# Kernel optimization log

Hardware: AMD Instinct MI355X
Metric: run time of the kernel (lower is better)

## Reference

```python
import jax, jax.numpy as jnp
import numpy as np

N_NODES = 50000
N_EDGES = 800000
IN_DIM = 128
HIDDEN = 128
N_GRAPHS = 64


def setup_inputs() -> dict:
    key = jax.random.key(0)
    ks = jax.random.split(key, 16)
    x = jax.random.normal(ks[0], (N_NODES, IN_DIM), dtype=jnp.float32)
    edge_index = jax.random.randint(ks[1], (2, N_EDGES), 0, N_NODES, dtype=jnp.int64)
    batch = jnp.sort(jax.random.randint(ks[2], (N_NODES,), 0, N_GRAPHS, dtype=jnp.int64))
    s = 1.0 / np.sqrt(IN_DIM)
    sh = 1.0 / np.sqrt(HIDDEN)
    return {
        "x": x,
        "edge_index": edge_index,
        "batch": batch,
        # SAGEConv1: lin_l (on aggregated neighbors, with bias), lin_r (on root, no bias)
        "w1l": jax.random.uniform(ks[3], (HIDDEN, IN_DIM), jnp.float32, -s, s),
        "b1l": jax.random.uniform(ks[4], (HIDDEN,), jnp.float32, -s, s),
        "w1r": jax.random.uniform(ks[5], (HIDDEN, IN_DIM), jnp.float32, -s, s),
        # SAGEConv2
        "w2l": jax.random.uniform(ks[6], (HIDDEN, HIDDEN), jnp.float32, -sh, sh),
        "b2l": jax.random.uniform(ks[7], (HIDDEN,), jnp.float32, -sh, sh),
        "w2r": jax.random.uniform(ks[8], (HIDDEN, HIDDEN), jnp.float32, -sh, sh),
        # MLP head
        "wl1": jax.random.uniform(ks[9], (64, HIDDEN), jnp.float32, -sh, sh),
        "bl1": jax.random.uniform(ks[10], (64,), jnp.float32, -sh, sh),
        "wout": jax.random.uniform(ks[11], (1, 64), jnp.float32, -0.125, 0.125),
        "bout": jax.random.uniform(ks[12], (1,), jnp.float32, -0.125, 0.125),
    }


def _sage_conv(x, src, dst, wl, bl, wr, n_nodes):
    # PyG SAGEConv (aggr='mean'): out = lin_l(mean_{j in N(i)} x_j) + lin_r(x_i)
    agg = jax.ops.segment_sum(x[src], dst, num_segments=n_nodes)  # [N, d]
    deg = jax.ops.segment_sum(jnp.ones_like(dst, dtype=x.dtype), dst, num_segments=n_nodes)
    agg = agg / jnp.maximum(deg, 1.0)[:, None]
    return agg @ wl.T + bl + x @ wr.T


def reference(x, edge_index, batch, w1l, b1l, w1r, w2l, b2l, w2r, wl1, bl1, wout, bout):
    src, dst = edge_index[0], edge_index[1]
    n = x.shape[0]
    h = jax.nn.relu(_sage_conv(x, src, dst, w1l, b1l, w1r, n))
    h = jax.nn.relu(_sage_conv(h, src, dst, w2l, b2l, w2r, n))
    # global_mean_pool over graph ids in `batch` -> [G, hidden]
    sums = jax.ops.segment_sum(h, batch, num_segments=N_GRAPHS)
    cnt = jax.ops.segment_sum(jnp.ones((n,), h.dtype), batch, num_segments=N_GRAPHS)
    g = sums / jnp.maximum(cnt, 1.0)[:, None]
    # MLP head (dropout is identity in eval mode)
    g = jax.nn.relu(g @ wl1.T + bl1)
    return jax.nn.sigmoid(g @ wout.T + bout)  # [G, 1]
```

## Files before the change

kernel.cpp:

```cpp
#include <hip/hip_runtime.h>
#include <cstdint>
#include <cstddef>

#define N_NODES  50000
#define N_EDGES  800000
#define DIM      128
#define N_GRAPHS 64
#define NB       98
#define BSH      9
#define EPB      2048
#define BPAD     16
#define CAP      16384

typedef __attribute__((ext_vector_type(8))) short     bf16x8;
typedef __attribute__((ext_vector_type(4))) float     f32x4;

__device__ __forceinline__ int clamp_node(int v) {
    return v < 0 ? 0 : (v >= N_NODES ? N_NODES - 1 : v);
}
__device__ __forceinline__ unsigned short f2bf(float f) {
    union { float f; unsigned u; } v; v.f = f;
    unsigned r = v.u + 0x7FFF + ((v.u >> 16) & 1);
    return (unsigned short)(r >> 16);
}
__device__ __forceinline__ float bflo(unsigned u) {
    union { unsigned u; float f; } v; v.u = u << 16; return v.f;
}
__device__ __forceinline__ float bfhi(unsigned u) {
    union { unsigned u; float f; } v; v.u = u & 0xFFFF0000u; return v.f;
}

__global__ __launch_bounds__(512) void k_bucket(const int* __restrict__ ei,
                                                int* __restrict__ bcur,
                                                unsigned* __restrict__ tmp) {
    __shared__ int cnt[128], cur[128], ofs[128];
    __shared__ int s[512];
    __shared__ unsigned list[EPB];
    int t = threadIdx.x;
    int base = blockIdx.x * EPB;
    int eend = base + EPB; if (eend > N_EDGES) eend = N_EDGES;

    if (t < 128) cnt[t] = 0;
    __syncthreads();

    int d[4], sv[4];
    bool ok[4];
    #pragma unroll
    for (int i = 0; i < 4; ++i) {
        int e = base + t + i * 512;
        ok[i] = (e < eend);
        if (ok[i]) {
            d[i]  = clamp_node(ei[N_EDGES + e]);
            sv[i] = clamp_node(ei[e]);
            atomicAdd(&cnt[d[i] >> BSH], 1);
        }
    }
    __syncthreads();
    int v = (t < 128) ? cnt[t] : 0;
    s[t] = v;
    __syncthreads();
    for (int off = 1; off < 128; off <<= 1) {
        int y = (t >= off && t < 128) ? s[t - off] : 0;
        __syncthreads();
        if (t < 128) s[t] += y;
        __syncthreads();
    }
    if (t < 128) { ofs[t] = s[t] - v; cur[t] = s[t] - v; }
    __syncthreads();
    #pragma unroll
    for (int i = 0; i < 4; ++i) {
        if (ok[i]) {
            int b = d[i] >> BSH;
            int p = atomicAdd(&cur[b], 1);
            list[p] = (unsigned)sv[i] | ((unsigned)(d[i] & 511) << 16);
        }
    }
    __syncthreads();
    int wv = t >> 6, lane = t & 63;
    const int NGRP = 13;
    for (int jj = 0; jj < NGRP; ++jj) {
        int b = wv + 8 * ((jj + (int)blockIdx.x) % NGRP);
        if (b >= NB) continue;
        int c = cnt[b];
        if (c == 0) continue;
        int gpos;
        if (lane == 0) gpos = atomicAdd(&bcur[b * BPAD], c);
        gpos = __shfl(gpos, 0);
        if (gpos + c > CAP) c = (gpos < CAP) ? (CAP - gpos) : 0;
        int ls = ofs[b];
        for (int i = lane; i < c; i += 64) tmp[b * CAP + gpos + i] = list[ls + i];
    }
}

__global__ __launch_bounds__(512) void k_csr(const unsigned* __restrict__ tmp,
                                             const int* __restrict__ bcur,
                                             int2* __restrict__ rsse,
                                             int* __restrict__ srcs) {
    __shared__ int lh[512], lcur[512];
    __shared__ int s[512];
    int b = blockIdx.x;
    int t = threadIdx.x;
    int base = b * CAP;
    int nc = bcur[b * BPAD];
    if (nc > CAP) nc = CAP;

    lh[t] = 0;
    __syncthreads();
    for (int e = t; e < nc; e += 512)
        atomicAdd(&lh[tmp[base + e] >> 16], 1);
    __syncthreads();
    int v = lh[t];
    s[t] = v;
    __syncthreads();
    for (int off = 1; off < 512; off <<= 1) {
        int y = (t >= off) ? s[t - off] : 0;
        __syncthreads();
        s[t] += y;
        __syncthreads();
    }
    int st = s[t] - v;
    lcur[t] = st;
    int node = (b << BSH) + t;
    if (node < N_NODES) rsse[node] = make_int2(base + st, base + st + v);
    __syncthreads();
    for (int e = t; e < nc; e += 512) {
        unsigned val = tmp[base + e];
        int pos = atomicAdd(&lcur[val >> 16], 1);
        srcs[base + pos] = (int)(val & 0xFFFFu);
    }
}

__global__ __launch_bounds__(256) void k_prep(const float* __restrict__ x,
                                              unsigned short* __restrict__ xb,
                                              const float* __restrict__ W1l,
                                              const float* __restrict__ W1r,
                                              const float* __restrict__ W2l,
                                              const float* __restrict__ W2r,
                                              unsigned short* __restrict__ wbuf1,
                                              unsigned short* __restrict__ wbuf2) {
    int i = blockIdx.x * 256 + threadIdx.x;
    const int n8 = N_NODES * 16;
    if (i < n8) {
        const float4* p = (const float4*)(x + (size_t)i * 8);
        float4 a = p[0], b = p[1];
        union { unsigned short s[8]; uint4 u; } o;
        o.s[0] = f2bf(a.x); o.s[1] = f2bf(a.y); o.s[2] = f2bf(a.z); o.s[3] = f2bf(a.w);
        o.s[4] = f2bf(b.x); o.s[5] = f2bf(b.y); o.s[6] = f2bf(b.z); o.s[7] = f2bf(b.w);
        *(uint4*)(xb + (size_t)i * 8) = o.u;
        return;
    }
    int tid = i - n8;
    if (tid >= 2 * 8 * 8 * 64) return;
    int which = tid >> 12;
    int id    = tid & 4095;
    const float* Wl = which ? W2l : W1l;
    const float* Wr = which ? W2r : W1r;
    unsigned short* wbuf = which ? wbuf2 : wbuf1;
    int lane = id & 63;
    int ks   = (id >> 6) & 7;
    int ot   = id >> 9;
    int o  = ot * 16 + (lane & 15);
    int kb = ks * 32 + ((lane >> 4) << 3);
    union { unsigned short s[8]; uint4 u; } frag;
    #pragma unroll
    for (int j = 0; j < 8; ++j) {
        int k = kb + j;
        float v = (k < DIM) ? Wl[o * DIM + k] : Wr[o * DIM + (k - DIM)];
        frag.s[j] = f2bf(v);
    }
    *(uint4*)(wbuf + (size_t)id * 8) = frag.u;
}

__global__ __launch_bounds__(256) void k_sage(const unsigned short* __restrict__ feat,
                                              const unsigned short* __restrict__ in2b,
                                              const int2* __restrict__ rsse,
                                              const int* __restrict__ srcs,
                                              const unsigned short* __restrict__ wbuf,
                                              const float* __restrict__ bias,
                                              unsigned short* __restrict__ outb) {
    __shared__ unsigned short almp[16][136];
    int t    = threadIdx.x;
    int wave = t >> 6;
    int lane = t & 63;
    int n0   = blockIdx.x * 16;

    bf16x8 B[2][8];
    #pragma unroll
    for (int ot = 0; ot < 2; ++ot)
        #pragma unroll
        for (int ks = 0; ks < 8; ++ks)
            B[ot][ks] = *(const bf16x8*)(wbuf +
                (((size_t)(wave * 2 + ot) * 8 + ks) * 64 + lane) * 8);

    {
        int q   = lane >> 4;
        int sub = lane & 15;
        int node  = n0 + wave * 4 + q;
        int2 se   = rsse[node];
        int start = se.x;
        int end   = se.y;
        float a0 = 0.f, a1 = 0.f, a2 = 0.f, a3 = 0.f;
        float a4 = 0.f, a5 = 0.f, a6 = 0.f, a7 = 0.f;
        const size_t coff = (size_t)sub * 8;

#define ACC8(r) { a0 += bflo(r.x); a1 += bfhi(r.x); a2 += bflo(r.y); a3 += bfhi(r.y); \
                  a4 += bflo(r.z); a5 += bfhi(r.z); a6 += bflo(r.w); a7 += bfhi(r.w); }
        int e = start;
        for (; e + 8 <= end; e += 8) {
            uint4 r0 = *(const uint4*)(feat + (size_t)srcs[e + 0] * DIM + coff);
            uint4 r1 = *(const uint4*)(feat + (size_t)srcs[e + 1] * DIM + coff);
            uint4 r2 = *(const uint4*)(feat + (size_t)srcs[e + 2] * DIM + coff);
            uint4 r3 = *(const uint4*)(feat + (size_t)srcs[e + 3] * DIM + coff);
            uint4 r4 = *(const uint4*)(feat + (size_t)srcs[e + 4] * DIM + coff);
            uint4 r5 = *(const uint4*)(feat + (size_t)srcs[e + 5] * DIM + coff);
            uint4 r6 = *(const uint4*)(feat + (size_t)srcs[e + 6] * DIM + coff);
            uint4 r7 = *(const uint4*)(feat + (size_t)srcs[e + 7] * DIM + coff);
            ACC8(r0) ACC8(r1) ACC8(r2) ACC8(r3) ACC8(r4) ACC8(r5) ACC8(r6) ACC8(r7)
        }
        for (; e + 2 <= end; e += 2) {
            uint4 r0 = *(const uint4*)(feat + (size_t)srcs[e + 0] * DIM + coff);
            uint4 r1 = *(const uint4*)(feat + (size_t)srcs[e + 1] * DIM + coff);
            ACC8(r0) ACC8(r1)
        }
        if (e < end) {
            uint4 r0 = *(const uint4*)(feat + (size_t)srcs[e] * DIM + coff);
            ACC8(r0)
        }
#undef ACC8
        float inv = 1.0f / fmaxf((float)(end - start), 1.0f);
        union { unsigned short s[8]; uint4 u; } o;
        o.s[0] = f2bf(a0 * inv); o.s[1] = f2bf(a1 * inv);
        o.s[2] = f2bf(a2 * inv); o.s[3] = f2bf(a3 * inv);
        o.s[4] = f2bf(a4 * inv); o.s[5] = f2bf(a5 * inv);
        o.s[6] = f2bf(a6 * inv); o.s[7] = f2bf(a7 * inv);
        *(uint4*)&almp[wave * 4 + q][sub * 8] = o.u;
    }
    __syncthreads();

    int row = lane & 15;
    int kl  = (lane >> 4) << 3;
    bf16x8 A[8];
    #pragma unroll
    for (int ks = 0; ks < 4; ++ks)
        A[ks] = *(const bf16x8*)&almp[row][kl + ks * 32];
    const unsigned short* xrow = in2b + (size_t)(n0 + row) * DIM + kl;
    #pragma unroll
    for (int ks = 0; ks < 4; ++ks)
        A[4 + ks] = *(const bf16x8*)(xrow + ks * 32);

    f32x4 acc0 = {0.f, 0.f, 0.f, 0.f}, acc1 = {0.f, 0.f, 0.f, 0.f};
    #pragma unroll
    for (int ks = 0; ks < 8; ++ks) {
        acc0 = __builtin_amdgcn_mfma_f32_16x16x32_bf16(A[ks], B[0][ks], acc0, 0, 0, 0);
        acc1 = __builtin_amdgcn_mfma_f32_16x16x32_bf16(A[ks], B[1][ks], acc1, 0, 0, 0);
    }

    int o0   = wave * 32;
    int ocol = lane & 15;
    int rb   = (lane >> 4) << 2;
    float b0 = bias[o0 + ocol];
    float b1 = bias[o0 + 16 + ocol];
    #pragma unroll
    for (int r = 0; r < 4; ++r) {
        size_t n = (size_t)(n0 + rb + r);
        outb[n * DIM + o0 + ocol]      = f2bf(fmaxf(acc0[r] + b0, 0.f));
        outb[n * DIM + o0 + 16 + ocol] = f2bf(fmaxf(acc1[r] + b1, 0.f));
    }
}

__global__ __launch_bounds__(256) void k_pool_partial(const unsigned short* __restrict__ h2,
                                                      const int* __restrict__ batch,
                                                      float* __restrict__ gsum) {
    int wid  = (blockIdx.x * 256 + threadIdx.x) >> 6;
    int lane = threadIdx.x & 63;
    int n0 = wid * 32;
    if (n0 >= N_NODES) return;
    int n1 = n0 + 32; if (n1 > N_NODES) n1 = N_NODES;
    int col = lane * 2;

    float ax = 0.f, ay = 0.f;
    int cur = batch[n0];
    for (int n = n0; n < n1; ++n) {
        int b = batch[n];
        if (b != cur) {
            atomicAdd(&gsum[cur * DIM + col], ax);
            atomicAdd(&gsum[cur * DIM + col + 1], ay);
            ax = 0.f; ay = 0.f; cur = b;
        }
        unsigned u = *(const unsigned*)(h2 + (size_t)n * DIM + col);
        ax += bflo(u); ay += bfhi(u);
    }
    atomicAdd(&gsum[cur * DIM + col], ax);
    atomicAdd(&gsum[cur * DIM + col + 1], ay);
}

__global__ __launch_bounds__(256) void k_head(const float* __restrict__ gsum,
                                              const int* __restrict__ batch,
                                              const float* __restrict__ wl1,
                                              const float* __restrict__ bl1,
                                              const float* __restrict__ wout,
                                              const float* __restrict__ bout,
                                              float* __restrict__ out) {
    int g = blockIdx.x;
    int t = threadIdx.x;

    int lo = 0, hi = N_NODES;
    while (lo < hi) { int mid = (lo + hi) >> 1; if (batch[mid] < g) lo = mid + 1; else hi = mid; }
    int s = lo;
    lo = 0; hi = N_NODES;
    while (lo < hi) { int mid = (lo + hi) >> 1; if (batch[mid] < g + 1) lo = mid + 1; else hi = mid; }
    int e = lo;

    __shared__ float gvec[DIM];
    if (t < DIM) {
        float cnt = fmaxf((float)(e - s), 1.0f);
        gvec[t] = gsum[g * DIM + t] / cnt;
    }
    __syncthreads();
    if (t < 64) {
        float a = bl1[t];
        #pragma unroll 4
        for (int k = 0; k < DIM; ++k) a += wl1[t * DIM + k] * gvec[k];
        float g1 = fmaxf(a, 0.f) * wout[t];
        #pragma unroll
        for (int off = 32; off > 0; off >>= 1) g1 += __shfl_down(g1, off);
        if (t == 0) {
            float z = g1 + bout[0];
            out[g] = 1.0f / (1.0f + expf(-z));
        }
    }
}

extern "C" void kernel_launch(void* const* d_in, const int* in_sizes, int n_in,
                              void* d_out, int out_size, void* d_ws, size_t ws_size,
                              hipStream_t stream) {
    const float* x     = (const float*)d_in[0];
    const int*   ei    = (const int*)d_in[1];
    const int*   batch = (const int*)d_in[2];
    const float* w1l   = (const float*)d_in[3];
    const float* b1l   = (const float*)d_in[4];
    const float* w1r   = (const float*)d_in[5];
    const float* w2l   = (const float*)d_in[6];
    const float* b2l   = (const float*)d_in[7];
    const float* w2r   = (const float*)d_in[8];
    const float* wl1   = (const float*)d_in[9];
    const float* bl1   = (const float*)d_in[10];
    const float* wout  = (const float*)d_in[11];
    const float* bout  = (const float*)d_in[12];
    float* out = (float*)d_out;

    char*  wsp = (char*)d_ws;
    size_t off = 0;
    auto alloc = [&](size_t bytes) -> char* {
        char* p = wsp + off;
        off += (bytes + 255) & ~(size_t)255;
        return p;
    };
    int*  bcur = (int*)alloc((size_t)NB * BPAD * 4);
    int2* rsse = (int2*)alloc((size_t)N_NODES * 8);
    int*  srcs = (int*)alloc((size_t)NB * CAP * 4);
    unsigned* tmp = (unsigned*)alloc((size_t)NB * CAP * 4);
    unsigned short* xb    = (unsigned short*)alloc((size_t)N_NODES * DIM * 2);
    unsigned short* h1b   = (unsigned short*)alloc((size_t)N_NODES * DIM * 2);
    unsigned short* h2b   = (unsigned short*)alloc((size_t)N_NODES * DIM * 2);
    unsigned short* wbuf1 = (unsigned short*)alloc((size_t)8 * 8 * 64 * 8 * 2);
    unsigned short* wbuf2 = (unsigned short*)alloc((size_t)8 * 8 * 64 * 8 * 2);
    float* gsum = (float*)alloc((size_t)N_GRAPHS * DIM * 4);

    hipMemsetAsync(bcur, 0, (size_t)NB * BPAD * 4, stream);
    hipMemsetAsync(gsum, 0, (size_t)N_GRAPHS * DIM * 4, stream);

    k_bucket<<<(N_EDGES + EPB - 1) / EPB, 512, 0, stream>>>(ei, bcur, tmp);
    k_csr<<<NB, 512, 0, stream>>>(tmp, bcur, rsse, srcs);

    k_prep<<<(N_NODES * 16 + 2 * 8 * 8 * 64 + 255) / 256, 256, 0, stream>>>(
        x, xb, w1l, w1r, w2l, w2r, wbuf1, wbuf2);

    k_sage<<<N_NODES / 16, 256, 0, stream>>>(xb, xb, rsse, srcs, wbuf1, b1l, h1b);
    k_sage<<<N_NODES / 16, 256, 0, stream>>>(h1b, h1b, rsse, srcs, wbuf2, b2l, h2b);
    k_pool_partial<<<(N_NODES + 127) / 128, 256, 0, stream>>>(h2b, batch, gsum);
    k_head<<<N_GRAPHS, 256, 0, stream>>>(gsum, batch, wl1, bl1, wout, bout, out);
}
```

Measured before the change: 158.0 us.

## Halve bucket size, deepen gather unroll, load weights lazily in SAGE kernel

Bucket width drops from 512 to 256 nodes, giving 196 buckets with 8192-entry capacity, so the CSR build runs twice as many blocks with smaller local histograms. The SAGE gather loop now loads 12 source indices up front and issues 12 independent row loads per iteration, to expose more memory-level parallelism. Weight fragments are no longer preloaded into 64 registers before the gather; they are loaded just before each MFMA. This cuts register pressure during the latency-bound gather and may raise occupancy, at the cost of weight loads on the GEMM critical path. A bucket holding more than 8192 edges would now be silently truncated.

```diff
diff --git a/kernel.cpp b/kernel.cpp
--- a/kernel.cpp
+++ b/kernel.cpp
@@ -6,11 +6,11 @@
 #define N_EDGES  800000
 #define DIM      128
 #define N_GRAPHS 64
-#define NB       98
-#define BSH      9
+#define NB       196
+#define BSH      8
 #define EPB      2048
 #define BPAD     16
-#define CAP      16384
+#define CAP      8192
 
 typedef __attribute__((ext_vector_type(8))) short     bf16x8;
 typedef __attribute__((ext_vector_type(4))) float     f32x4;
@@ -33,14 +33,14 @@
 __global__ __launch_bounds__(512) void k_bucket(const int* __restrict__ ei,
                                                 int* __restrict__ bcur,
                                                 unsigned* __restrict__ tmp) {
-    __shared__ int cnt[128], cur[128], ofs[128];
+    __shared__ int cnt[256], cur[256], ofs[256];
     __shared__ int s[512];
     __shared__ unsigned list[EPB];
     int t = threadIdx.x;
     int base = blockIdx.x * EPB;
     int eend = base + EPB; if (eend > N_EDGES) eend = N_EDGES;
 
-    if (t < 128) cnt[t] = 0;
+    if (t < 256) cnt[t] = 0;
     __syncthreads();
 
     int d[4], sv[4];
@@ -56,28 +56,28 @@
         }
     }
     __syncthreads();
-    int v = (t < 128) ? cnt[t] : 0;
+    int v = (t < 256) ? cnt[t] : 0;
     s[t] = v;
     __syncthreads();
-    for (int off = 1; off < 128; off <<= 1) {
-        int y = (t >= off && t < 128) ? s[t - off] : 0;
+    for (int off = 1; off < 256; off <<= 1) {
+        int y = (t >= off && t < 256) ? s[t - off] : 0;
         __syncthreads();
-        if (t < 128) s[t] += y;
+        if (t < 256) s[t] += y;
         __syncthreads();
     }
-    if (t < 128) { ofs[t] = s[t] - v; cur[t] = s[t] - v; }
+    if (t < 256) { ofs[t] = s[t] - v; cur[t] = s[t] - v; }
     __syncthreads();
     #pragma unroll
     for (int i = 0; i < 4; ++i) {
         if (ok[i]) {
             int b = d[i] >> BSH;
             int p = atomicAdd(&cur[b], 1);
-            list[p] = (unsigned)sv[i] | ((unsigned)(d[i] & 511) << 16);
+            list[p] = (unsigned)sv[i] | ((unsigned)(d[i] & 255) << 16);
         }
     }
     __syncthreads();
     int wv = t >> 6, lane = t & 63;
-    const int NGRP = 13;
+    const int NGRP = 25;
     for (int jj = 0; jj < NGRP; ++jj) {
         int b = wv + 8 * ((jj + (int)blockIdx.x) % NGRP);
         if (b >= NB) continue;
@@ -96,7 +96,7 @@
                                              const int* __restrict__ bcur,
                                              int2* __restrict__ rsse,
                                              int* __restrict__ srcs) {
-    __shared__ int lh[512], lcur[512];
+    __shared__ int lh[256], lcur[256];
     __shared__ int s[512];
     int b = blockIdx.x;
     int t = threadIdx.x;
@@ -104,24 +104,26 @@
     int nc = bcur[b * BPAD];
     if (nc > CAP) nc = CAP;
 
-    lh[t] = 0;
+    if (t < 256) lh[t] = 0;
     __syncthreads();
     for (int e = t; e < nc; e += 512)
         atomicAdd(&lh[tmp[base + e] >> 16], 1);
     __syncthreads();
-    int v = lh[t];
+    int v = (t < 256) ? lh[t] : 0;
     s[t] = v;
     __syncthreads();
-    for (int off = 1; off < 512; off <<= 1) {
-        int y = (t >= off) ? s[t - off] : 0;
+    for (int off = 1; off < 256; off <<= 1) {
+        int y = (t >= off && t < 256) ? s[t - off] : 0;
         __syncthreads();
-        s[t] += y;
+        if (t < 256) s[t] += y;
         __syncthreads();
     }
-    int st = s[t] - v;
-    lcur[t] = st;
-    int node = (b << BSH) + t;
-    if (node < N_NODES) rsse[node] = make_int2(base + st, base + st + v);
+    if (t < 256) {
+        int st = s[t] - v;
+        lcur[t] = st;
+        int node = (b << BSH) + t;
+        if (node < N_NODES) rsse[node] = make_int2(base + st, base + st + v);
+    }
     __syncthreads();
     for (int e = t; e < nc; e += 512) {
         unsigned val = tmp[base + e];
@@ -184,14 +186,6 @@
     int lane = t & 63;
     int n0   = blockIdx.x * 16;
 
-    bf16x8 B[2][8];
-    #pragma unroll
-    for (int ot = 0; ot < 2; ++ot)
-        #pragma unroll
-        for (int ks = 0; ks < 8; ++ks)
-            B[ot][ks] = *(const bf16x8*)(wbuf +
-                (((size_t)(wave * 2 + ot) * 8 + ks) * 64 + lane) * 8);
-
     {
         int q   = lane >> 4;
         int sub = lane & 15;
@@ -206,23 +200,34 @@
 #define ACC8(r) { a0 += bflo(r.x); a1 += bfhi(r.x); a2 += bflo(r.y); a3 += bfhi(r.y); \
                   a4 += bflo(r.z); a5 += bfhi(r.z); a6 += bflo(r.w); a7 += bfhi(r.w); }
         int e = start;
-        for (; e + 8 <= end; e += 8) {
+        for (; e + 12 <= end; e += 12) {
+            int s0 = srcs[e + 0], s1 = srcs[e + 1], s2 = srcs[e + 2];
+            int s3 = srcs[e + 3], s4 = srcs[e + 4], s5 = srcs[e + 5];
+            int s6 = srcs[e + 6], s7 = srcs[e + 7], s8 = srcs[e + 8];
+            int s9 = srcs[e + 9], s10 = srcs[e + 10], s11 = srcs[e + 11];
+            uint4 r0  = *(const uint4*)(feat + (size_t)s0  * DIM + coff);
+            uint4 r1  = *(const uint4*)(feat + (size_t)s1  * DIM + coff);
+            uint4 r2  = *(const uint4*)(feat + (size_t)s2  * DIM + coff);
+            uint4 r3  = *(const uint4*)(feat + (size_t)s3  * DIM + coff);
+            uint4 r4  = *(const uint4*)(feat + (size_t)s4  * DIM + coff);
+            uint4 r5  = *(const uint4*)(feat + (size_t)s5  * DIM + coff);
+            uint4 r6  = *(const uint4*)(feat + (size_t)s6  * DIM + coff);
+            uint4 r7  = *(const uint4*)(feat + (size_t)s7  * DIM + coff);
+            uint4 r8  = *(const uint4*)(feat + (size_t)s8  * DIM + coff);
+            uint4 r9  = *(const uint4*)(feat + (size_t)s9  * DIM + coff);
+            uint4 r10 = *(const uint4*)(feat + (size_t)s10 * DIM + coff);
+            uint4 r11 = *(const uint4*)(feat + (size_t)s11 * DIM + coff);
+            ACC8(r0) ACC8(r1) ACC8(r2) ACC8(r3) ACC8(r4) ACC8(r5)
+            ACC8(r6) ACC8(r7) ACC8(r8) ACC8(r9) ACC8(r10) ACC8(r11)
+        }
+        for (; e + 4 <= end; e += 4) {
             uint4 r0 = *(const uint4*)(feat + (size_t)srcs[e + 0] * DIM + coff);
             uint4 r1 = *(const uint4*)(feat + (size_t)srcs[e + 1] * DIM + coff);
             uint4 r2 = *(const uint4*)(feat + (size_t)srcs[e + 2] * DIM + coff);
             uint4 r3 = *(const uint4*)(feat + (size_t)srcs[e + 3] * DIM + coff);
-            uint4 r4 = *(const uint4*)(feat + (size_t)srcs[e + 4] * DIM + coff);
-            uint4 r5 = *(const uint4*)(feat + (size_t)srcs[e + 5] * DIM + coff);
-            uint4 r6 = *(const uint4*)(feat + (size_t)srcs[e + 6] * DIM + coff);
-            uint4 r7 = *(const uint4*)(feat + (size_t)srcs[e + 7] * DIM + coff);
-            ACC8(r0) ACC8(r1) ACC8(r2) ACC8(r3) ACC8(r4) ACC8(r5) ACC8(r6) ACC8(r7)
-        }
-        for (; e + 2 <= end; e += 2) {
-            uint4 r0 = *(const uint4*)(feat + (size_t)srcs[e + 0] * DIM + coff);
-            uint4 r1 = *(const uint4*)(feat + (size_t)srcs[e + 1] * DIM + coff);
-            ACC8(r0) ACC8(r1)
-        }
-        if (e < end) {
+            ACC8(r0) ACC8(r1) ACC8(r2) ACC8(r3)
+        }
+        for (; e < end; ++e) {
             uint4 r0 = *(const uint4*)(feat + (size_t)srcs[e] * DIM + coff);
             ACC8(r0)
         }
@@ -248,11 +253,15 @@
     for (int ks = 0; ks < 4; ++ks)
         A[4 + ks] = *(const bf16x8*)(xrow + ks * 32);
 
+    const unsigned short* wb0 = wbuf + ((size_t)(wave * 2)     * 8 * 64 + lane) * 8;
+    const unsigned short* wb1 = wbuf + ((size_t)(wave * 2 + 1) * 8 * 64 + lane) * 8;
     f32x4 acc0 = {0.f, 0.f, 0.f, 0.f}, acc1 = {0.f, 0.f, 0.f, 0.f};
     #pragma unroll
     for (int ks = 0; ks < 8; ++ks) {
-        acc0 = __builtin_amdgcn_mfma_f32_16x16x32_bf16(A[ks], B[0][ks], acc0, 0, 0, 0);
-        acc1 = __builtin_amdgcn_mfma_f32_16x16x32_bf16(A[ks], B[1][ks], acc1, 0, 0, 0);
+        bf16x8 b0 = *(const bf16x8*)(wb0 + (size_t)ks * 64 * 8);
+        bf16x8 b1 = *(const bf16x8*)(wb1 + (size_t)ks * 64 * 8);
+        acc0 = __builtin_amdgcn_mfma_f32_16x16x32_bf16(A[ks], b0, acc0, 0, 0, 0);
+        acc1 = __builtin_amdgcn_mfma_f32_16x16x32_bf16(A[ks], b1, acc1, 0, 0, 0);
     }
 
     int o0   = wave * 32;
```

Result: no change. 157.7 us (-0.2%).
